# Kernel optimization log

Hardware: AMD Instinct MI355X
Metric: run time of the kernel (lower is better)

The kernel has to match this reference:

```python
import jax, jax.numpy as jnp
import numpy as np

NSTEPS = 64  # Euler integration steps for the CPAB ODE solve


def cpab_basis_1d(nC):
    """Null-space basis of the continuity constraints for a 1D CPAB
    tessellation with nC cells (velocity a_c*x + b_c per cell, continuous
    at interior knots, no zero-boundary constraint). Returns [2*nC, nC+1]."""
    d = 2 * nC
    L = np.zeros((nC - 1, d), dtype=np.float64)
    for k in range(1, nC):  # small fixed loop over cells
        xk = k / nC
        L[k - 1, 2 * (k - 1):2 * k] = [xk, 1.0]
        L[k - 1, 2 * k:2 * k + 2] = [-xk, -1.0]
    _, _, Vt = np.linalg.svd(L)
    return np.ascontiguousarray(Vt[nC - 1:].T).astype(np.float32)  # [2nC, nC+1]


def setup_inputs() -> dict:
    key = jax.random.key(0)
    k1, k2 = jax.random.split(key)
    B, Lin, C, nC = 256, 2048, 32, 32
    x = jax.random.normal(k1, (B, Lin, C), dtype=jnp.float32)
    theta = 0.5 * jax.random.normal(k2, (B, nC + 1), dtype=jnp.float32)
    basis = jnp.asarray(cpab_basis_1d(nC))  # [64, 33]
    return {"x": x, "theta": theta, "basis": basis, "out_len": 2048}


def reference(x, theta, basis, out_len):
    # x: [B, Lin, C]; theta: [B, d]; basis: [2*nC, d]
    B, Lin, C = x.shape
    nC = basis.shape[0] // 2
    dt = 1.0 / NSTEPS

    # Per-cell affine velocity coefficients: v_c(x) = a_c * x + b_c
    A = jnp.einsum('kd,bd->bk', basis, theta).reshape(B, nC, 2)
    Aa, Ab = A[..., 0], A[..., 1]  # each [B, nC]

    # Integrate dphi/dt = v(phi) from the uniform grid on [0,1]
    grid = jnp.linspace(0.0, 1.0, out_len, dtype=x.dtype)
    phi0 = jnp.broadcast_to(grid, (B, out_len))

    def step(phi, _):
        idx = jnp.clip(jnp.floor(phi * nC).astype(jnp.int32), 0, nC - 1)
        a = jnp.take_along_axis(Aa, idx, axis=1)
        b = jnp.take_along_axis(Ab, idx, axis=1)
        return phi + (a * phi + b) * dt, None

    phi, _ = jax.lax.scan(step, phi0, None, length=NSTEPS)

    # Linear resampling of x at the warped grid
    p = jnp.clip(phi, 0.0, 1.0) * (Lin - 1)           # [B, out_len]
    i0 = jnp.clip(jnp.floor(p).astype(jnp.int32), 0, Lin - 2)
    w = (p - i0.astype(p.dtype))[..., None]           # [B, out_len, 1]
    g0 = jnp.take_along_axis(x, i0[..., None], axis=1)        # [B, out_len, C]
    g1 = jnp.take_along_axis(x, (i0 + 1)[..., None], axis=1)  # [B, out_len, C]
    return g0 * (1.0 - w) + g1 * w
```

## Files before the change

kernel.cpp:

```cpp
#include <hip/hip_runtime.h>


#define NSTEPS 64
#define NC     32
#define DD     33
#define LIN    2048
#define CCH    32
#define OUTLEN 2048
#define JPB    256

__global__ __launch_bounds__(256) void cpab_warp_kernel(
    const float* __restrict__ x,
    const float* __restrict__ theta,
    const float* __restrict__ basis,
    float* __restrict__ out)
{
    __shared__ float Asm[2 * NC];
    __shared__ int   i0s[JPB];
    __shared__ float ws[JPB];

    const int t = threadIdx.x;
    const int blocksPerB = OUTLEN / JPB;
    const int b     = blockIdx.x / blocksPerB;
    const int jbase = (blockIdx.x % blocksPerB) * JPB;

    if (t < 2 * NC) {
        const float* bs = basis + t * DD;
        const float* th = theta + b * DD;
        float acc = 0.0f;
        #pragma unroll
        for (int d = 0; d < DD; ++d) acc = fmaf(bs[d], th[d], acc);
        Asm[t] = acc;
    }
    __syncthreads();

    {
        const int j = jbase + t;
        float phi = (float)j * (1.0f / (float)(OUTLEN - 1));
        const float dt = 1.0f / (float)NSTEPS;
        const float2* Ac = (const float2*)Asm;
        #pragma unroll 8
        for (int s = 0; s < NSTEPS; ++s) {
            int idx = (int)floorf(phi * (float)NC);
            idx = min(max(idx, 0), NC - 1);
            float2 ab = Ac[idx];
            phi = fmaf(fmaf(ab.x, phi, ab.y), dt, phi);
        }
        float p = fminf(fmaxf(phi, 0.0f), 1.0f) * (float)(LIN - 1);
        int i0 = (int)floorf(p);
        i0 = min(max(i0, 0), LIN - 2);
        i0s[t] = i0;
        ws[t]  = p - (float)i0;
    }
    __syncthreads();

    const float* xb = x + (size_t)b * (LIN * CCH);
    float* ob = out + ((size_t)b * OUTLEN + jbase) * CCH;
    const int c   = t & (CCH - 1);
    const int jl0 = t >> 5;
    #pragma unroll 4
    for (int it = 0; it < (JPB * CCH) / 256; ++it) {
        int   jl = it * 8 + jl0;
        int   i0 = i0s[jl];
        float w  = ws[jl];
        float g0 = xb[i0 * CCH + c];
        float g1 = xb[(i0 + 1) * CCH + c];
        ob[jl * CCH + c] = fmaf(w, g1 - g0, g0);
    }
}

extern "C" void kernel_launch(void* const* d_in, const int* in_sizes, int n_in,
                              void* d_out, int out_size, void* d_ws, size_t ws_size,
                              hipStream_t stream) {
    const float* x     = (const float*)d_in[0];
    const float* theta = (const float*)d_in[1];
    const float* basis = (const float*)d_in[2];
    float* out = (float*)d_out;

    const int B = in_sizes[1] / DD;
    const int grid = B * (OUTLEN / JPB);
    cpab_warp_kernel<<<grid, 256, 0, stream>>>(x, theta, basis, out);
}
```

Before: 29.38 us.

## Make each wave self-contained, drop block syncs, vectorize gather with float4

Each 64-lane wave now computes the per-cell velocity coefficients itself, using shuffles into a per-wave LDS table. This removes both __syncthreads barriers and lets waves progress independently. The table stores precomputed (1+a*dt, b*dt), so each Euler step is one FMA, and the 64-step loop is fully unrolled. The gather/lerp phase uses float4 loads and stores. The cost is redundant coefficient computation in every wave, and it relies on LDS write/read visibility within a wave without an explicit barrier.

After: 29.40 us. Within noise of the previous version (+0.1%).

```diff
diff --git a/kernel.cpp b/kernel.cpp
--- a/kernel.cpp
+++ b/kernel.cpp
@@ -7,7 +7,9 @@
 #define LIN    2048
 #define CCH    32
 #define OUTLEN 2048
-#define JPB    256
+#define JPW    64
+#define WPB    4
+#define JPB    (JPW * WPB)
 
 __global__ __launch_bounds__(256) void cpab_warp_kernel(
     const float* __restrict__ x,
@@ -15,57 +17,65 @@
     const float* __restrict__ basis,
     float* __restrict__ out)
 {
-    __shared__ float Asm[2 * NC];
-    __shared__ int   i0s[JPB];
-    __shared__ float ws[JPB];
+    __shared__ float2 ctab[WPB][NC];
+    __shared__ float2 iw[WPB][JPW];
 
-    const int t = threadIdx.x;
+    const int t    = threadIdx.x;
+    const int wave = t >> 6;
+    const int lane = t & 63;
     const int blocksPerB = OUTLEN / JPB;
     const int b     = blockIdx.x / blocksPerB;
-    const int jbase = (blockIdx.x % blocksPerB) * JPB;
+    const int jbase = (blockIdx.x % blocksPerB) * JPB + wave * JPW;
 
-    if (t < 2 * NC) {
-        const float* bs = basis + t * DD;
+    const float dt = 1.0f / (float)NSTEPS;
+
+    float acc = 0.0f;
+    {
+        const float* bs = basis + lane * DD;
         const float* th = theta + b * DD;
-        float acc = 0.0f;
         #pragma unroll
         for (int d = 0; d < DD; ++d) acc = fmaf(bs[d], th[d], acc);
-        Asm[t] = acc;
     }
-    __syncthreads();
+    {
+        int c = lane & (NC - 1);
+        float a  = __shfl(acc, 2 * c);
+        float bb = __shfl(acc, 2 * c + 1);
+        if (lane < NC) ctab[wave][c] = make_float2(fmaf(a, dt, 1.0f), bb * dt);
+    }
 
     {
-        const int j = jbase + t;
+        const int j = jbase + lane;
         float phi = (float)j * (1.0f / (float)(OUTLEN - 1));
-        const float dt = 1.0f / (float)NSTEPS;
-        const float2* Ac = (const float2*)Asm;
-        #pragma unroll 8
+        const float2* ct = ctab[wave];
+        #pragma unroll
         for (int s = 0; s < NSTEPS; ++s) {
-            int idx = (int)floorf(phi * (float)NC);
-            idx = min(max(idx, 0), NC - 1);
-            float2 ab = Ac[idx];
-            phi = fmaf(fmaf(ab.x, phi, ab.y), dt, phi);
+            float f = fminf(fmaxf(phi * (float)NC, 0.0f), (float)(NC - 1));
+            float2 cc = ct[(int)f];
+            phi = fmaf(cc.x, phi, cc.y);
         }
         float p = fminf(fmaxf(phi, 0.0f), 1.0f) * (float)(LIN - 1);
-        int i0 = (int)floorf(p);
-        i0 = min(max(i0, 0), LIN - 2);
-        i0s[t] = i0;
-        ws[t]  = p - (float)i0;
+        int i0 = min(max((int)p, 0), LIN - 2);
+        iw[wave][lane] = make_float2(p - (float)i0, (float)i0);
     }
-    __syncthreads();
 
-    const float* xb = x + (size_t)b * (LIN * CCH);
-    float* ob = out + ((size_t)b * OUTLEN + jbase) * CCH;
-    const int c   = t & (CCH - 1);
-    const int jl0 = t >> 5;
-    #pragma unroll 4
-    for (int it = 0; it < (JPB * CCH) / 256; ++it) {
-        int   jl = it * 8 + jl0;
-        int   i0 = i0s[jl];
-        float w  = ws[jl];
-        float g0 = xb[i0 * CCH + c];
-        float g1 = xb[(i0 + 1) * CCH + c];
-        ob[jl * CCH + c] = fmaf(w, g1 - g0, g0);
+    const float4* xb = (const float4*)(x + (size_t)b * (LIN * CCH));
+    float4* ob = (float4*)(out + ((size_t)b * OUTLEN + jbase) * CCH);
+    const int c4  = lane & 7;
+    const int jl0 = lane >> 3;
+    #pragma unroll
+    for (int it = 0; it < JPW / 8; ++it) {
+        int jl = it * 8 + jl0;
+        float2 f = iw[wave][jl];
+        int   i0 = (int)f.y;
+        float w  = f.x;
+        float4 g0 = xb[i0 * (CCH / 4) + c4];
+        float4 g1 = xb[(i0 + 1) * (CCH / 4) + c4];
+        float4 r;
+        r.x = fmaf(w, g1.x - g0.x, g0.x);
+        r.y = fmaf(w, g1.y - g0.y, g0.y);
+        r.z = fmaf(w, g1.z - g0.z, g0.z);
+        r.w = fmaf(w, g1.w - g0.w, g0.w);
+        ob[jl * (CCH / 4) + c4] = r;
     }
 }
 
```
